# Kernel optimization log

Hardware: AMD Instinct MI355X
Metric: run time of the kernel (lower is better)

Reference implementation:

```python
import jax, jax.numpy as jnp
import numpy as np

N, E, H, C = 100000, 1600000, 4, 32  # nodes, edges, heads, per-head channels
F_IN, F_HID, F_OUT = 128, 32, 16
NEG_SLOPE = 0.2


def setup_inputs() -> dict:
    key = jax.random.key(0)
    ks = jax.random.split(key, 16)
    s = 0.05
    return {
        "x": jax.random.normal(ks[0], (N, F_IN), jnp.float32),
        "edge_index": jax.random.randint(ks[1], (2, E), 0, N, jnp.int32),
        "W0": jax.random.normal(ks[2], (F_IN, H * C), jnp.float32) * s,
        "att_src0": jax.random.normal(ks[3], (H, C), jnp.float32) * s,
        "att_dst0": jax.random.normal(ks[4], (H, C), jnp.float32) * s,
        "b0": jax.random.normal(ks[5], (H * C,), jnp.float32) * s,
        "W1": jax.random.normal(ks[6], (H * C, H * C), jnp.float32) * s,
        "att_src1": jax.random.normal(ks[7], (H, C), jnp.float32) * s,
        "att_dst1": jax.random.normal(ks[8], (H, C), jnp.float32) * s,
        "b1": jax.random.normal(ks[9], (H * C,), jnp.float32) * s,
        "Wm1": jax.random.normal(ks[10], (H * C, F_HID), jnp.float32) * s,
        "bm1": jax.random.normal(ks[11], (F_HID,), jnp.float32) * s,
        "Wm2": jax.random.normal(ks[12], (F_HID, F_OUT), jnp.float32) * s,
        "bm2": jax.random.normal(ks[13], (F_OUT,), jnp.float32) * s,
    }


def gat_layer(x, src, dst, W, att_src, att_dst, bias):
    n = x.shape[0]
    h = (x @ W).reshape(n, H, C)                       # [N,H,C]
    a_src = jnp.einsum("nhc,hc->nh", h, att_src)       # [N,H]
    a_dst = jnp.einsum("nhc,hc->nh", h, att_dst)       # [N,H]
    e = a_src[src] + a_dst[dst]                        # [E,H]
    e = jnp.where(e > 0, e, NEG_SLOPE * e)             # leaky_relu(0.2)
    m = jax.ops.segment_max(e, dst, num_segments=n)    # [N,H] segment softmax
    ee = jnp.exp(e - m[dst])
    z = jax.ops.segment_sum(ee, dst, num_segments=n)
    alpha = ee / z[dst]                                # [E,H]
    msg = alpha[:, :, None] * h[src]                   # [E,H,C]
    out = jax.ops.segment_sum(msg, dst, num_segments=n)  # [N,H,C]
    return out.reshape(n, H * C) + bias


def reference(x, edge_index, W0, att_src0, att_dst0, b0,
              W1, att_src1, att_dst1, b1, Wm1, bm1, Wm2, bm2):
    src, dst = edge_index[0], edge_index[1]
    x = jax.nn.relu(gat_layer(x, src, dst, W0, att_src0, att_dst0, b0))
    x = jax.nn.relu(gat_layer(x, src, dst, W1, att_src1, att_dst1, b1))
    x = jax.nn.relu(x @ Wm1 + bm1)
    return x @ Wm2 + bm2
```

## Files before the change

kernel.cpp:

```cpp
#include <hip/hip_runtime.h>
#include <hip/hip_bf16.h>

#define NEG 0.2f

typedef __attribute__((ext_vector_type(8))) short short8v;
typedef __attribute__((ext_vector_type(4))) float f32x4;

static __device__ __forceinline__ float bf2f(unsigned int u16){
  return __uint_as_float(u16 << 16);
}
static __device__ __forceinline__ unsigned short f2bf(float f){
  __hip_bfloat16 h = __float2bfloat16(f);
  return *reinterpret_cast<unsigned short*>(&h);
}

#define CHUNK 2048
#define PER_T 8


static __device__ __forceinline__ void bcount_body(
    const int* __restrict__ dst, int* __restrict__ bcnt, int E, int NB,
    int blk, int* lc)
{
  int t = threadIdx.x;
  int ebase = blk * CHUNK;
  for (int j=t; j<NB; j+=256) lc[j]=0;
  __syncthreads();
  #pragma unroll
  for (int k=0;k<PER_T;++k){
    int i = ebase + t + k*256;
    if (i < E) atomicAdd(&lc[dst[i] >> 8], 1);
  }
  __syncthreads();
  for (int j=t; j<NB; j+=256){
    int c = lc[j];
    if (c) atomicAdd(&bcnt[j], c);
  }
}

static __device__ __forceinline__ void binpass_body(
    const int* __restrict__ src, const int* __restrict__ dst,
    int* __restrict__ bfill, unsigned int* __restrict__ pairs, int E, int NB,
    int blk, int* lcnt, int* lbase)
{
  int t = threadIdx.x;
  int ebase = blk * CHUNK;
  for (int j=t; j<NB; j+=256) lcnt[j]=0;
  __syncthreads();
  unsigned int pv[PER_T]; int pb[PER_T];
  #pragma unroll
  for (int k=0;k<PER_T;++k){
    int i = ebase + t + k*256;
    pb[k] = -1;
    if (i < E){
      int d = dst[i];
      int s = src[i];
      pb[k] = d >> 8;
      pv[k] = ((unsigned int)s << 8) | (unsigned int)(d & 255);
      atomicAdd(&lcnt[pb[k]], 1);
    }
  }
  __syncthreads();
  for (int j=t; j<NB; j+=256){
    int c = lcnt[j];
    lbase[j] = c ? atomicAdd(&bfill[j], c) : 0;
    lcnt[j] = 0;
  }
  __syncthreads();
  #pragma unroll
  for (int k=0;k<PER_T;++k){
    if (pb[k] >= 0){
      int ofs = atomicAdd(&lcnt[pb[k]], 1);
      pairs[lbase[pb[k]] + ofs] = pv[k];
    }
  }
}

template<int IN_BF16>
static __device__ __forceinline__ void gemm_att_body(
    const void* __restrict__ xin_, const unsigned short* __restrict__ wt,
    const float* __restrict__ atts, const float* __restrict__ attd,
    unsigned short* __restrict__ hb, float* __restrict__ as_, float* __restrict__ ad_,
    int n, int blk, unsigned short* xls)
{
  int t = threadIdx.x;
  int base = blk*64;
  int nrem = n - base;
  if (IN_BF16){
    const uint4* Xb = reinterpret_cast<const uint4*>(xin_);
    #pragma unroll
    for (int j=0;j<4;++j){
      int i = t + j*256;
      int row = i >> 4, c16 = i & 15;
      uint4 v = (row < nrem) ? Xb[(size_t)(base+row)*16 + c16]
                             : make_uint4(0,0,0,0);
      int addr = row*256 + ((c16*16) ^ ((row&7)<<4));
      *reinterpret_cast<uint4*>(reinterpret_cast<char*>(xls) + addr) = v;
    }
  } else {
    const float4* X4 = reinterpret_cast<const float4*>(xin_);
    #pragma unroll
    for (int j=0;j<8;++j){
      int i = t + j*256;
      int row = i >> 5, cb = i & 31;
      float4 v = (row < nrem) ? X4[(size_t)(base+row)*32 + cb] : make_float4(0.f,0.f,0.f,0.f);
      unsigned int p0 = (unsigned int)f2bf(v.x) | ((unsigned int)f2bf(v.y)<<16);
      unsigned int p1 = (unsigned int)f2bf(v.z) | ((unsigned int)f2bf(v.w)<<16);
      int addr = row*256 + ((cb*8) ^ ((row&7)<<4));
      *reinterpret_cast<uint2*>(reinterpret_cast<char*>(xls) + addr) = make_uint2(p0,p1);
    }
  }
  __syncthreads();
  int w = t >> 6;
  int l = t & 63;
  int l15 = l & 15, l4 = l >> 4;
  int n0 = w*32;
  short8v bfr[2][4];
  #pragma unroll
  for (int nt=0;nt<2;++nt){
    const unsigned short* bp = wt + (size_t)(n0 + nt*16 + l15)*128 + l4*8;
    #pragma unroll
    for (int kk=0;kk<4;++kk)
      bfr[nt][kk] = *reinterpret_cast<const short8v*>(bp + kk*32);
  }
  f32x4 acc[4][2];
  #pragma unroll
  for (int mt=0;mt<4;++mt)
    #pragma unroll
    for (int nt=0;nt<2;++nt)
      acc[mt][nt] = (f32x4){0.f,0.f,0.f,0.f};
  #pragma unroll
  for (int kk=0;kk<4;++kk){
    short8v afr[4];
    #pragma unroll
    for (int mt=0;mt<4;++mt){
      int row = mt*16 + l15;
      int addr = row*256 + ((kk*64 + l4*16) ^ ((row&7)<<4));
      afr[mt] = *reinterpret_cast<const short8v*>(reinterpret_cast<char*>(xls) + addr);
    }
    #pragma unroll
    for (int mt=0;mt<4;++mt)
      #pragma unroll
      for (int nt=0;nt<2;++nt)
        acc[mt][nt] = __builtin_amdgcn_mfma_f32_16x16x32_bf16(afr[mt], bfr[nt][kk], acc[mt][nt], 0, 0, 0);
  }
  float av0 = atts[n0 + l15],    av1 = atts[n0 + 16 + l15];
  float dv0 = attd[n0 + l15],    dv1 = attd[n0 + 16 + l15];
  #pragma unroll
  for (int mt=0;mt<4;++mt){
    #pragma unroll
    for (int r=0;r<4;++r){
      float ps = acc[mt][0][r]*av0 + acc[mt][1][r]*av1;
      float pd = acc[mt][0][r]*dv0 + acc[mt][1][r]*dv1;
      ps += __shfl_xor(ps,1); ps += __shfl_xor(ps,2);
      ps += __shfl_xor(ps,4); ps += __shfl_xor(ps,8);
      pd += __shfl_xor(pd,1); pd += __shfl_xor(pd,2);
      pd += __shfl_xor(pd,4); pd += __shfl_xor(pd,8);
      int node = base + mt*16 + l4*4 + r;
      if (l15==0 && node < n){
        as_[node*4 + w] = ps;
        ad_[node*4 + w] = pd;
      }
    }
  }
  __syncthreads();
  #pragma unroll
  for (int mt=0;mt<4;++mt)
    #pragma unroll
    for (int nt=0;nt<2;++nt)
      #pragma unroll
      for (int r=0;r<4;++r){
        int row = mt*16 + l4*4 + r;
        int col = n0 + nt*16 + l15;
        xls[row*128 + col] = f2bf(acc[mt][nt][r]);
      }
  __syncthreads();
  const uint4* xsrc = reinterpret_cast<const uint4*>(xls);
  uint4* hdst = reinterpret_cast<uint4*>(hb + (size_t)base*128);
  #pragma unroll
  for (int j=0;j<4;++j){
    int i = t + j*256;
    int row = i >> 4;
    if (row < nrem) hdst[i] = xsrc[i];
  }
}


__global__ __launch_bounds__(256) void k_wconv_bcount(
    const float* __restrict__ W0, const float* __restrict__ W1,
    unsigned short* __restrict__ wt0, unsigned short* __restrict__ wt1,
    const int* __restrict__ dst, int* __restrict__ bcnt, int E, int NB)
{
  __shared__ int lc[512];
  int b = blockIdx.x;
  if (b < 128){
    const float* W = (b < 64) ? W0 : W1;
    unsigned short* wt = (b < 64) ? wt0 : wt1;
    int i = (b & 63)*256 + threadIdx.x;
    int k = i >> 7, nn = i & 127;
    wt[nn*128 + k] = f2bf(W[i]);
  } else {
    bcount_body(dst, bcnt, E, NB, b - 128, lc);
  }
}

__global__ __launch_bounds__(256) void k_bscan(
    const int* __restrict__ bcnt, int* __restrict__ bstart,
    int* __restrict__ bfill, int NB)
{
  __shared__ int sd[256];
  int t = threadIdx.x;
  int i0 = 2*t, i1 = 2*t+1;
  int v0 = (i0<NB) ? bcnt[i0] : 0;
  int v1 = (i1<NB) ? bcnt[i1] : 0;
  int s = v0+v1;
  sd[t]=s; __syncthreads();
  for (int off=1; off<256; off<<=1){
    int x = (t>=off) ? sd[t-off] : 0;
    __syncthreads();
    sd[t] += x;
    __syncthreads();
  }
  int ex = sd[t]-s;
  if (i0<=NB){ bstart[i0]=ex; if(i0<NB) bfill[i0]=ex; }
  ex += v0;
  if (i1<=NB){ bstart[i1]=ex; if(i1<NB) bfill[i1]=ex; }
}

__global__ __launch_bounds__(256) void k_gemm1_binpass(
    const float* __restrict__ xin, const unsigned short* __restrict__ wt,
    const float* __restrict__ atts, const float* __restrict__ attd,
    unsigned short* __restrict__ hb, float* __restrict__ as_, float* __restrict__ ad_,
    int n, int nG,
    const int* __restrict__ src, const int* __restrict__ dst,
    int* __restrict__ bfill, unsigned int* __restrict__ pairs, int E, int NB)
{
  __shared__ __align__(16) unsigned short xls[64*128];
  __shared__ int lcnt[512];
  __shared__ int lbase[512];
  int b = blockIdx.x;
  if (b < nG){
    gemm_att_body<0>(xin, wt, atts, attd, hb, as_, ad_, n, b, xls);
  } else {
    binpass_body(src, dst, bfill, pairs, E, NB, b - nG, lcnt, lbase);
  }
}

__global__ __launch_bounds__(256) void k_gemm2(
    const unsigned short* __restrict__ xin, const unsigned short* __restrict__ wt,
    const float* __restrict__ atts, const float* __restrict__ attd,
    unsigned short* __restrict__ hb, float* __restrict__ as_, float* __restrict__ ad_, int n)
{
  __shared__ __align__(16) unsigned short xls[64*128];
  gemm_att_body<1>(xin, wt, atts, attd, hb, as_, ad_, n, blockIdx.x, xls);
}

__global__ __launch_bounds__(256) void k_csr(
    const unsigned int* __restrict__ pairs, const int* __restrict__ bstart,
    int* __restrict__ rowptr, int* __restrict__ csr, int n)
{
  __shared__ int lc[256];
  __shared__ int sd[256];
  __shared__ int rp[257];
  int b = blockIdx.x;
  int base = b << 8;
  int t = threadIdx.x;
  int cnt = n - base; if (cnt > 256) cnt = 256;
  int beg = bstart[b], end = bstart[b+1];
  lc[t]=0; __syncthreads();
  for (int i = beg + t; i < end; i += 256)
    atomicAdd(&lc[pairs[i] & 255u], 1);
  __syncthreads();
  int v = lc[t];
  sd[t]=v; __syncthreads();
  for (int off=1; off<256; off<<=1){
    int x = (t>=off) ? sd[t-off] : 0;
    __syncthreads();
    sd[t] += x;
    __syncthreads();
  }
  rp[t+1] = beg + sd[t];
  if (t==0) rp[0] = beg;
  lc[t] = 0;
  __syncthreads();
  if (t < cnt) rowptr[base + t] = rp[t];
  if (t==0 && base + cnt == n) rowptr[n] = rp[cnt];
  for (int i = beg + t; i < end; i += 256){
    unsigned int p = pairs[i];
    int d = (int)(p & 255u);
    int ofs = atomicAdd(&lc[d], 1);
    csr[rp[d] + ofs] = (int)(p >> 8);
  }
}

__global__ __launch_bounds__(256) void k_aggr(
    const unsigned short* __restrict__ hb, const float* __restrict__ as_,
    const float* __restrict__ ad_, const int* __restrict__ rowptr,
    const int* __restrict__ csr, const float* __restrict__ bias,
    unsigned short* __restrict__ out, int n)
{
  int wid = (int)((blockIdx.x*(size_t)blockDim.x + threadIdx.x) >> 6);
  int lane = threadIdx.x & 63;
  if (wid >= n) return;
  int half = lane >> 5;
  int li   = lane & 31;
  int c0   = li*4;
  int head = li >> 3;
  float adn = ad_[wid*4 + head];
  int beg = rowptr[wid], end = rowptr[wid+1];
  int deg = end - beg;
  float4 acc = make_float4(0.f,0.f,0.f,0.f);
  float z = 0.f;
  int nfull = deg & ~7;
  int lim = beg + nfull;
  int i = beg + half*4;
  int s0=0,s1=0,s2=0,s3=0;
  if (i < lim){ s0=csr[i]; s1=csr[i+1]; s2=csr[i+2]; s3=csr[i+3]; }
  for (; i < lim; ){
    int ni = i + 8;
    int t0=0,t1=0,t2=0,t3=0;
    if (ni < lim){ t0=csr[ni]; t1=csr[ni+1]; t2=csr[ni+2]; t3=csr[ni+3]; }
    float e0 = as_[s0*4+head];
    float e1 = as_[s1*4+head];
    float e2 = as_[s2*4+head];
    float e3 = as_[s3*4+head];
    uint2 p0 = *reinterpret_cast<const uint2*>(hb + (size_t)s0*128 + c0);
    uint2 p1 = *reinterpret_cast<const uint2*>(hb + (size_t)s1*128 + c0);
    uint2 p2 = *reinterpret_cast<const uint2*>(hb + (size_t)s2*128 + c0);
    uint2 p3 = *reinterpret_cast<const uint2*>(hb + (size_t)s3*128 + c0);
    e0 += adn; e1 += adn; e2 += adn; e3 += adn;
    e0 = (e0>0.f)?e0:NEG*e0;
    e1 = (e1>0.f)?e1:NEG*e1;
    e2 = (e2>0.f)?e2:NEG*e2;
    e3 = (e3>0.f)?e3:NEG*e3;
    float x0 = __expf(e0);
    float x1 = __expf(e1);
    float x2 = __expf(e2);
    float x3 = __expf(e3);
    z += (x0+x1)+(x2+x3);
    acc.x = fmaf(x0, bf2f(p0.x & 0xffffu), acc.x);
    acc.y = fmaf(x0, bf2f(p0.x >> 16),     acc.y);
    acc.z = fmaf(x0, bf2f(p0.y & 0xffffu), acc.z);
    acc.w = fmaf(x0, bf2f(p0.y >> 16),     acc.w);
    acc.x = fmaf(x1, bf2f(p1.x & 0xffffu), acc.x);
    acc.y = fmaf(x1, bf2f(p1.x >> 16),     acc.y);
    acc.z = fmaf(x1, bf2f(p1.y & 0xffffu), acc.z);
    acc.w = fmaf(x1, bf2f(p1.y >> 16),     acc.w);
    acc.x = fmaf(x2, bf2f(p2.x & 0xffffu), acc.x);
    acc.y = fmaf(x2, bf2f(p2.x >> 16),     acc.y);
    acc.z = fmaf(x2, bf2f(p2.y & 0xffffu), acc.z);
    acc.w = fmaf(x2, bf2f(p2.y >> 16),     acc.w);
    acc.x = fmaf(x3, bf2f(p3.x & 0xffffu), acc.x);
    acc.y = fmaf(x3, bf2f(p3.x >> 16),     acc.y);
    acc.z = fmaf(x3, bf2f(p3.y & 0xffffu), acc.z);
    acc.w = fmaf(x3, bf2f(p3.y >> 16),     acc.w);
    i = ni; s0=t0; s1=t1; s2=t2; s3=t3;
  }
  for (int j = beg + nfull + half; j < end; j += 2){
    int s = csr[j];
    float e = as_[s*4+head] + adn;
    e = (e>0.f)?e:NEG*e;
    float ee = __expf(e);
    z += ee;
    uint2 pv = *reinterpret_cast<const uint2*>(hb + (size_t)s*128 + c0);
    acc.x = fmaf(ee, bf2f(pv.x & 0xffffu), acc.x);
    acc.y = fmaf(ee, bf2f(pv.x >> 16),     acc.y);
    acc.z = fmaf(ee, bf2f(pv.y & 0xffffu), acc.z);
    acc.w = fmaf(ee, bf2f(pv.y >> 16),     acc.w);
  }
  z     += __shfl_xor(z, 32);
  acc.x += __shfl_xor(acc.x, 32);
  acc.y += __shfl_xor(acc.y, 32);
  acc.z += __shfl_xor(acc.z, 32);
  acc.w += __shfl_xor(acc.w, 32);
  if (half == 0){
    float4 o;
    if (deg > 0){
      float rz = 1.f/z;
      o.x = fmaxf(fmaf(acc.x,rz,bias[c0  ]), 0.f);
      o.y = fmaxf(fmaf(acc.y,rz,bias[c0+1]), 0.f);
      o.z = fmaxf(fmaf(acc.z,rz,bias[c0+2]), 0.f);
      o.w = fmaxf(fmaf(acc.w,rz,bias[c0+3]), 0.f);
    } else {
      o.x = fmaxf(bias[c0  ], 0.f);
      o.y = fmaxf(bias[c0+1], 0.f);
      o.z = fmaxf(bias[c0+2], 0.f);
      o.w = fmaxf(bias[c0+3], 0.f);
    }
    unsigned int lo = (unsigned int)f2bf(o.x) | ((unsigned int)f2bf(o.y)<<16);
    unsigned int hi = (unsigned int)f2bf(o.z) | ((unsigned int)f2bf(o.w)<<16);
    *reinterpret_cast<uint2*>(out + (size_t)wid*128 + c0) = make_uint2(lo,hi);
  }
}

__global__ __launch_bounds__(256) void k_mlp(
    const unsigned short* __restrict__ xb, const float* __restrict__ Wm1, const float* __restrict__ bm1,
    const float* __restrict__ Wm2, const float* __restrict__ bm2,
    float* __restrict__ out, int n)
{
  __shared__ float xs[64*129];
  __shared__ float w1s[128*32];
  __shared__ float hs[64*33];
  __shared__ float w2s[32*16];
  __shared__ float b1s[32];
  __shared__ float b2s[16];
  int t = threadIdx.x;
  int base = blockIdx.x*64;
  const uint4* Xb = reinterpret_cast<const uint4*>(xb);
  #pragma unroll
  for (int j=0;j<4;++j){
    int i = t + j*256;
    int row = i >> 4, seg = i & 15;
    uint4 v = (base+row < n) ? Xb[(size_t)(base+row)*16 + seg] : make_uint4(0,0,0,0);
    float* xp = &xs[row*129 + seg*8];
    xp[0] = bf2f(v.x & 0xffffu); xp[1] = bf2f(v.x >> 16);
    xp[2] = bf2f(v.y & 0xffffu); xp[3] = bf2f(v.y >> 16);
    xp[4] = bf2f(v.z & 0xffffu); xp[5] = bf2f(v.z >> 16);
    xp[6] = bf2f(v.w & 0xffffu); xp[7] = bf2f(v.w >> 16);
  }
  for (int i=t; i<128*32; i+=256) w1s[i]=Wm1[i];
  for (int i=t; i<32*16;  i+=256) w2s[i]=Wm2[i];
  if (t<32) b1s[t]=bm1[t];
  if (t<16) b2s[t]=bm2[t];
  __syncthreads();
  int l = t&63, g = t>>6;
  float hid[8];
  #pragma unroll
  for (int j=0;j<8;++j) hid[j]=0.f;
  for (int k=0;k<128;++k){
    float xk = xs[l*129+k];
    #pragma unroll
    for (int j=0;j<8;++j) hid[j] = fmaf(xk, w1s[k*32 + g*8 + j], hid[j]);
  }
  #pragma unroll
  for (int j=0;j<8;++j) hs[l*33 + g*8 + j] = fmaxf(hid[j] + b1s[g*8+j], 0.f);
  __syncthreads();
  float o[4] = {0.f,0.f,0.f,0.f};
  for (int k=0;k<32;++k){
    float xv = hs[l*33+k];
    #pragma unroll
    for (int j=0;j<4;++j) o[j] = fmaf(xv, w2s[k*16 + g*4 + j], o[j]);
  }
  int node = base + l;
  if (node < n){
    #pragma unroll
    for (int j=0;j<4;++j) out[(size_t)node*16 + g*4 + j] = o[j] + b2s[g*4+j];
  }
}

extern "C" void kernel_launch(void* const* d_in, const int* in_sizes, int n_in,
                              void* d_out, int out_size, void* d_ws, size_t ws_size,
                              hipStream_t stream)
{
  const float* x   = (const float*)d_in[0];
  const int*   ei  = (const int*)  d_in[1];
  const float* W0  = (const float*)d_in[2];
  const float* as0 = (const float*)d_in[3];
  const float* ad0 = (const float*)d_in[4];
  const float* b0  = (const float*)d_in[5];
  const float* W1  = (const float*)d_in[6];
  const float* as1 = (const float*)d_in[7];
  const float* ad1 = (const float*)d_in[8];
  const float* b1  = (const float*)d_in[9];
  const float* Wm1 = (const float*)d_in[10];
  const float* bm1 = (const float*)d_in[11];
  const float* Wm2 = (const float*)d_in[12];
  const float* bm2 = (const float*)d_in[13];
  int N = in_sizes[0]/128;
  int E = in_sizes[1]/2;
  const int* srcI = ei;
  const int* dstI = ei + E;

  char* ws = (char*)d_ws;
  size_t off = 0;
  auto alloc = [&](size_t bytes)->void*{
    void* p = ws + off; off += (bytes + 255) & ~(size_t)255; return p;
  };
  unsigned short* hbuf = (unsigned short*)alloc((size_t)N*128*2);
  unsigned short* xbuf = (unsigned short*)alloc((size_t)N*128*2);
  float* asb   = (float*)alloc((size_t)N*4*4);
  float* adb   = (float*)alloc((size_t)N*4*4);
  int* rowptr  = (int*)alloc((size_t)(N+1)*4);
  int* bcnt    = (int*)alloc(2048);
  int* bstart  = (int*)alloc(2052);
  int* bfill   = (int*)alloc(2048);
  int* csr     = (int*)alloc((size_t)E*4);
  unsigned int* pairs = (unsigned int*)alloc((size_t)E*4);
  unsigned short* wt0 = (unsigned short*)alloc(128*128*2);
  unsigned short* wt1 = (unsigned short*)alloc(128*128*2);
  (void)ws_size; (void)n_in; (void)out_size;

  int NB = (N + 255) >> 8;
  int gC = (E + CHUNK - 1) / CHUNK;
  int gG = (N+63)/64;
  int gA = (int)(((size_t)N*64 + 255)/256);

  hipMemsetAsync(bcnt, 0, 2048, stream);
  k_wconv_bcount<<<128+gC,256,0,stream>>>(W0, W1, wt0, wt1, dstI, bcnt, E, NB);
  k_bscan       <<<1,256,0,stream>>>(bcnt, bstart, bfill, NB);
  k_gemm1_binpass<<<gG+gC,256,0,stream>>>(x, wt0, as0, ad0, hbuf, asb, adb, N, gG,
                                          srcI, dstI, bfill, pairs, E, NB);
  k_csr         <<<NB,256,0,stream>>>(pairs, bstart, rowptr, csr, N);
  k_aggr        <<<gA,256,0,stream>>>(hbuf, asb, adb, rowptr, csr, b0, xbuf, N);
  k_gemm2       <<<gG,256,0,stream>>>(xbuf, wt1, as1, ad1, hbuf, asb, adb, N);
  k_aggr        <<<gA,256,0,stream>>>(hbuf, asb, adb, rowptr, csr, b1, xbuf, N);
  k_mlp         <<<gG,256,0,stream>>>(xbuf, Wm1, bm1, Wm2, bm2, (float*)d_out, N);
}
```

Baseline: 286.9 us.

## Fuse GAT aggregation with following GEMM and with the MLP head

Layer-1 aggregation is fused with the layer-2 GEMM and attention projection, and layer-2 aggregation is fused with the two-layer MLP. Each block of 64 nodes aggregates into shared memory and then runs the next stage in place. This removes two launches and two round-trips of the intermediate N×128 bf16 buffer through global memory. The cost is fewer waves in flight for the latency-bound gather (64 nodes per 256-thread block done serially, 16 rows per wave) plus separate h/a buffers per layer. The MLP now reads its weights straight from global instead of staging them in LDS.

Result: slower. 362.8 us (+26.4%).

```diff
diff --git a/kernel.cpp b/kernel.cpp
--- a/kernel.cpp
+++ b/kernel.cpp
@@ -16,7 +16,6 @@
 
 #define CHUNK 2048
 #define PER_T 8
-
 
 static __device__ __forceinline__ void bcount_body(
     const int* __restrict__ dst, int* __restrict__ bcnt, int E, int NB,
@@ -76,241 +75,14 @@
   }
 }
 
-template<int IN_BF16>
-static __device__ __forceinline__ void gemm_att_body(
-    const void* __restrict__ xin_, const unsigned short* __restrict__ wt,
-    const float* __restrict__ atts, const float* __restrict__ attd,
-    unsigned short* __restrict__ hb, float* __restrict__ as_, float* __restrict__ ad_,
-    int n, int blk, unsigned short* xls)
-{
-  int t = threadIdx.x;
-  int base = blk*64;
-  int nrem = n - base;
-  if (IN_BF16){
-    const uint4* Xb = reinterpret_cast<const uint4*>(xin_);
-    #pragma unroll
-    for (int j=0;j<4;++j){
-      int i = t + j*256;
-      int row = i >> 4, c16 = i & 15;
-      uint4 v = (row < nrem) ? Xb[(size_t)(base+row)*16 + c16]
-                             : make_uint4(0,0,0,0);
-      int addr = row*256 + ((c16*16) ^ ((row&7)<<4));
-      *reinterpret_cast<uint4*>(reinterpret_cast<char*>(xls) + addr) = v;
-    }
-  } else {
-    const float4* X4 = reinterpret_cast<const float4*>(xin_);
-    #pragma unroll
-    for (int j=0;j<8;++j){
-      int i = t + j*256;
-      int row = i >> 5, cb = i & 31;
-      float4 v = (row < nrem) ? X4[(size_t)(base+row)*32 + cb] : make_float4(0.f,0.f,0.f,0.f);
-      unsigned int p0 = (unsigned int)f2bf(v.x) | ((unsigned int)f2bf(v.y)<<16);
-      unsigned int p1 = (unsigned int)f2bf(v.z) | ((unsigned int)f2bf(v.w)<<16);
-      int addr = row*256 + ((cb*8) ^ ((row&7)<<4));
-      *reinterpret_cast<uint2*>(reinterpret_cast<char*>(xls) + addr) = make_uint2(p0,p1);
-    }
-  }
-  __syncthreads();
-  int w = t >> 6;
-  int l = t & 63;
-  int l15 = l & 15, l4 = l >> 4;
-  int n0 = w*32;
-  short8v bfr[2][4];
-  #pragma unroll
-  for (int nt=0;nt<2;++nt){
-    const unsigned short* bp = wt + (size_t)(n0 + nt*16 + l15)*128 + l4*8;
-    #pragma unroll
-    for (int kk=0;kk<4;++kk)
-      bfr[nt][kk] = *reinterpret_cast<const short8v*>(bp + kk*32);
-  }
-  f32x4 acc[4][2];
-  #pragma unroll
-  for (int mt=0;mt<4;++mt)
-    #pragma unroll
-    for (int nt=0;nt<2;++nt)
-      acc[mt][nt] = (f32x4){0.f,0.f,0.f,0.f};
-  #pragma unroll
-  for (int kk=0;kk<4;++kk){
-    short8v afr[4];
-    #pragma unroll
-    for (int mt=0;mt<4;++mt){
-      int row = mt*16 + l15;
-      int addr = row*256 + ((kk*64 + l4*16) ^ ((row&7)<<4));
-      afr[mt] = *reinterpret_cast<const short8v*>(reinterpret_cast<char*>(xls) + addr);
-    }
-    #pragma unroll
-    for (int mt=0;mt<4;++mt)
-      #pragma unroll
-      for (int nt=0;nt<2;++nt)
-        acc[mt][nt] = __builtin_amdgcn_mfma_f32_16x16x32_bf16(afr[mt], bfr[nt][kk], acc[mt][nt], 0, 0, 0);
-  }
-  float av0 = atts[n0 + l15],    av1 = atts[n0 + 16 + l15];
-  float dv0 = attd[n0 + l15],    dv1 = attd[n0 + 16 + l15];
-  #pragma unroll
-  for (int mt=0;mt<4;++mt){
-    #pragma unroll
-    for (int r=0;r<4;++r){
-      float ps = acc[mt][0][r]*av0 + acc[mt][1][r]*av1;
-      float pd = acc[mt][0][r]*dv0 + acc[mt][1][r]*dv1;
-      ps += __shfl_xor(ps,1); ps += __shfl_xor(ps,2);
-      ps += __shfl_xor(ps,4); ps += __shfl_xor(ps,8);
-      pd += __shfl_xor(pd,1); pd += __shfl_xor(pd,2);
-      pd += __shfl_xor(pd,4); pd += __shfl_xor(pd,8);
-      int node = base + mt*16 + l4*4 + r;
-      if (l15==0 && node < n){
-        as_[node*4 + w] = ps;
-        ad_[node*4 + w] = pd;
-      }
-    }
-  }
-  __syncthreads();
-  #pragma unroll
-  for (int mt=0;mt<4;++mt)
-    #pragma unroll
-    for (int nt=0;nt<2;++nt)
-      #pragma unroll
-      for (int r=0;r<4;++r){
-        int row = mt*16 + l4*4 + r;
-        int col = n0 + nt*16 + l15;
-        xls[row*128 + col] = f2bf(acc[mt][nt][r]);
-      }
-  __syncthreads();
-  const uint4* xsrc = reinterpret_cast<const uint4*>(xls);
-  uint4* hdst = reinterpret_cast<uint4*>(hb + (size_t)base*128);
-  #pragma unroll
-  for (int j=0;j<4;++j){
-    int i = t + j*256;
-    int row = i >> 4;
-    if (row < nrem) hdst[i] = xsrc[i];
-  }
-}
-
-
-__global__ __launch_bounds__(256) void k_wconv_bcount(
-    const float* __restrict__ W0, const float* __restrict__ W1,
-    unsigned short* __restrict__ wt0, unsigned short* __restrict__ wt1,
-    const int* __restrict__ dst, int* __restrict__ bcnt, int E, int NB)
-{
-  __shared__ int lc[512];
-  int b = blockIdx.x;
-  if (b < 128){
-    const float* W = (b < 64) ? W0 : W1;
-    unsigned short* wt = (b < 64) ? wt0 : wt1;
-    int i = (b & 63)*256 + threadIdx.x;
-    int k = i >> 7, nn = i & 127;
-    wt[nn*128 + k] = f2bf(W[i]);
-  } else {
-    bcount_body(dst, bcnt, E, NB, b - 128, lc);
-  }
-}
-
-__global__ __launch_bounds__(256) void k_bscan(
-    const int* __restrict__ bcnt, int* __restrict__ bstart,
-    int* __restrict__ bfill, int NB)
-{
-  __shared__ int sd[256];
-  int t = threadIdx.x;
-  int i0 = 2*t, i1 = 2*t+1;
-  int v0 = (i0<NB) ? bcnt[i0] : 0;
-  int v1 = (i1<NB) ? bcnt[i1] : 0;
-  int s = v0+v1;
-  sd[t]=s; __syncthreads();
-  for (int off=1; off<256; off<<=1){
-    int x = (t>=off) ? sd[t-off] : 0;
-    __syncthreads();
-    sd[t] += x;
-    __syncthreads();
-  }
-  int ex = sd[t]-s;
-  if (i0<=NB){ bstart[i0]=ex; if(i0<NB) bfill[i0]=ex; }
-  ex += v0;
-  if (i1<=NB){ bstart[i1]=ex; if(i1<NB) bfill[i1]=ex; }
-}
-
-__global__ __launch_bounds__(256) void k_gemm1_binpass(
-    const float* __restrict__ xin, const unsigned short* __restrict__ wt,
-    const float* __restrict__ atts, const float* __restrict__ attd,
-    unsigned short* __restrict__ hb, float* __restrict__ as_, float* __restrict__ ad_,
-    int n, int nG,
-    const int* __restrict__ src, const int* __restrict__ dst,
-    int* __restrict__ bfill, unsigned int* __restrict__ pairs, int E, int NB)
-{
-  __shared__ __align__(16) unsigned short xls[64*128];
-  __shared__ int lcnt[512];
-  __shared__ int lbase[512];
-  int b = blockIdx.x;
-  if (b < nG){
-    gemm_att_body<0>(xin, wt, atts, attd, hb, as_, ad_, n, b, xls);
-  } else {
-    binpass_body(src, dst, bfill, pairs, E, NB, b - nG, lcnt, lbase);
-  }
-}
-
-__global__ __launch_bounds__(256) void k_gemm2(
-    const unsigned short* __restrict__ xin, const unsigned short* __restrict__ wt,
-    const float* __restrict__ atts, const float* __restrict__ attd,
-    unsigned short* __restrict__ hb, float* __restrict__ as_, float* __restrict__ ad_, int n)
-{
-  __shared__ __align__(16) unsigned short xls[64*128];
-  gemm_att_body<1>(xin, wt, atts, attd, hb, as_, ad_, n, blockIdx.x, xls);
-}
-
-__global__ __launch_bounds__(256) void k_csr(
-    const unsigned int* __restrict__ pairs, const int* __restrict__ bstart,
-    int* __restrict__ rowptr, int* __restrict__ csr, int n)
-{
-  __shared__ int lc[256];
-  __shared__ int sd[256];
-  __shared__ int rp[257];
-  int b = blockIdx.x;
-  int base = b << 8;
-  int t = threadIdx.x;
-  int cnt = n - base; if (cnt > 256) cnt = 256;
-  int beg = bstart[b], end = bstart[b+1];
-  lc[t]=0; __syncthreads();
-  for (int i = beg + t; i < end; i += 256)
-    atomicAdd(&lc[pairs[i] & 255u], 1);
-  __syncthreads();
-  int v = lc[t];
-  sd[t]=v; __syncthreads();
-  for (int off=1; off<256; off<<=1){
-    int x = (t>=off) ? sd[t-off] : 0;
-    __syncthreads();
-    sd[t] += x;
-    __syncthreads();
-  }
-  rp[t+1] = beg + sd[t];
-  if (t==0) rp[0] = beg;
-  lc[t] = 0;
-  __syncthreads();
-  if (t < cnt) rowptr[base + t] = rp[t];
-  if (t==0 && base + cnt == n) rowptr[n] = rp[cnt];
-  for (int i = beg + t; i < end; i += 256){
-    unsigned int p = pairs[i];
-    int d = (int)(p & 255u);
-    int ofs = atomicAdd(&lc[d], 1);
-    csr[rp[d] + ofs] = (int)(p >> 8);
-  }
-}
-
-__global__ __launch_bounds__(256) void k_aggr(
+static __device__ __forceinline__ float4 aggr_partial(
     const unsigned short* __restrict__ hb, const float* __restrict__ as_,
-    const float* __restrict__ ad_, const int* __restrict__ rowptr,
-    const int* __restrict__ csr, const float* __restrict__ bias,
-    unsigned short* __restrict__ out, int n)
-{
-  int wid = (int)((blockIdx.x*(size_t)blockDim.x + threadIdx.x) >> 6);
-  int lane = threadIdx.x & 63;
-  if (wid >= n) return;
-  int half = lane >> 5;
-  int li   = lane & 31;
-  int c0   = li*4;
-  int head = li >> 3;
-  float adn = ad_[wid*4 + head];
-  int beg = rowptr[wid], end = rowptr[wid+1];
-  int deg = end - beg;
+    float adn, const int* __restrict__ csr, int beg, int end,
+    int half, int head, int c0, float& zref)
+{
   float4 acc = make_float4(0.f,0.f,0.f,0.f);
   float z = 0.f;
+  int deg = end - beg;
   int nfull = deg & ~7;
   int lim = beg + nfull;
   int i = beg + half*4;
@@ -368,83 +140,447 @@
     acc.z = fmaf(ee, bf2f(pv.y & 0xffffu), acc.z);
     acc.w = fmaf(ee, bf2f(pv.y >> 16),     acc.w);
   }
-  z     += __shfl_xor(z, 32);
-  acc.x += __shfl_xor(acc.x, 32);
-  acc.y += __shfl_xor(acc.y, 32);
-  acc.z += __shfl_xor(acc.z, 32);
-  acc.w += __shfl_xor(acc.w, 32);
-  if (half == 0){
-    float4 o;
-    if (deg > 0){
-      float rz = 1.f/z;
-      o.x = fmaxf(fmaf(acc.x,rz,bias[c0  ]), 0.f);
-      o.y = fmaxf(fmaf(acc.y,rz,bias[c0+1]), 0.f);
-      o.z = fmaxf(fmaf(acc.z,rz,bias[c0+2]), 0.f);
-      o.w = fmaxf(fmaf(acc.w,rz,bias[c0+3]), 0.f);
-    } else {
-      o.x = fmaxf(bias[c0  ], 0.f);
-      o.y = fmaxf(bias[c0+1], 0.f);
-      o.z = fmaxf(bias[c0+2], 0.f);
-      o.w = fmaxf(bias[c0+3], 0.f);
-    }
-    unsigned int lo = (unsigned int)f2bf(o.x) | ((unsigned int)f2bf(o.y)<<16);
-    unsigned int hi = (unsigned int)f2bf(o.z) | ((unsigned int)f2bf(o.w)<<16);
-    *reinterpret_cast<uint2*>(out + (size_t)wid*128 + c0) = make_uint2(lo,hi);
-  }
-}
-
-__global__ __launch_bounds__(256) void k_mlp(
-    const unsigned short* __restrict__ xb, const float* __restrict__ Wm1, const float* __restrict__ bm1,
+  zref = z;
+  return acc;
+}
+
+template<int IN_BF16>
+static __device__ __forceinline__ void gemm_att_body(
+    const void* __restrict__ xin_, const unsigned short* __restrict__ wt,
+    const float* __restrict__ atts, const float* __restrict__ attd,
+    unsigned short* __restrict__ hb, float* __restrict__ as_, float* __restrict__ ad_,
+    int n, int blk, unsigned short* xls)
+{
+  int t = threadIdx.x;
+  int base = blk*64;
+  int nrem = n - base;
+  if (IN_BF16){
+    const uint4* Xb = reinterpret_cast<const uint4*>(xin_);
+    #pragma unroll
+    for (int j=0;j<4;++j){
+      int i = t + j*256;
+      int row = i >> 4, c16 = i & 15;
+      uint4 v = (row < nrem) ? Xb[(size_t)(base+row)*16 + c16]
+                             : make_uint4(0,0,0,0);
+      int addr = row*256 + ((c16*16) ^ ((row&7)<<4));
+      *reinterpret_cast<uint4*>(reinterpret_cast<char*>(xls) + addr) = v;
+    }
+  } else {
+    const float4* X4 = reinterpret_cast<const float4*>(xin_);
+    #pragma unroll
+    for (int j=0;j<8;++j){
+      int i = t + j*256;
+      int row = i >> 5, cb = i & 31;
+      float4 v = (row < nrem) ? X4[(size_t)(base+row)*32 + cb] : make_float4(0.f,0.f,0.f,0.f);
+      unsigned int p0 = (unsigned int)f2bf(v.x) | ((unsigned int)f2bf(v.y)<<16);
+      unsigned int p1 = (unsigned int)f2bf(v.z) | ((unsigned int)f2bf(v.w)<<16);
+      int addr = row*256 + ((cb*8) ^ ((row&7)<<4));
+      *reinterpret_cast<uint2*>(reinterpret_cast<char*>(xls) + addr) = make_uint2(p0,p1);
+    }
+  }
+  __syncthreads();
+  int w = t >> 6;
+  int l = t & 63;
+  int l15 = l & 15, l4 = l >> 4;
+  int n0 = w*32;
+  short8v bfr[2][4];
+  #pragma unroll
+  for (int nt=0;nt<2;++nt){
+    const unsigned short* bp = wt + (size_t)(n0 + nt*16 + l15)*128 + l4*8;
+    #pragma unroll
+    for (int kk=0;kk<4;++kk)
+      bfr[nt][kk] = *reinterpret_cast<const short8v*>(bp + kk*32);
+  }
+  f32x4 acc[4][2];
+  #pragma unroll
+  for (int mt=0;mt<4;++mt)
+    #pragma unroll
+    for (int nt=0;nt<2;++nt)
+      acc[mt][nt] = (f32x4){0.f,0.f,0.f,0.f};
+  #pragma unroll
+  for (int kk=0;kk<4;++kk){
+    short8v afr[4];
+    #pragma unroll
+    for (int mt=0;mt<4;++mt){
+      int row = mt*16 + l15;
+      int addr = row*256 + ((kk*64 + l4*16) ^ ((row&7)<<4));
+      afr[mt] = *reinterpret_cast<const short8v*>(reinterpret_cast<char*>(xls) + addr);
+    }
+    #pragma unroll
+    for (int mt=0;mt<4;++mt)
+      #pragma unroll
+      for (int nt=0;nt<2;++nt)
+        acc[mt][nt] = __builtin_amdgcn_mfma_f32_16x16x32_bf16(afr[mt], bfr[nt][kk], acc[mt][nt], 0, 0, 0);
+  }
+  float av0 = atts[n0 + l15],    av1 = atts[n0 + 16 + l15];
+  float dv0 = attd[n0 + l15],    dv1 = attd[n0 + 16 + l15];
+  #pragma unroll
+  for (int mt=0;mt<4;++mt){
+    #pragma unroll
+    for (int r=0;r<4;++r){
+      float ps = acc[mt][0][r]*av0 + acc[mt][1][r]*av1;
+      float pd = acc[mt][0][r]*dv0 + acc[mt][1][r]*dv1;
+      ps += __shfl_xor(ps,1); ps += __shfl_xor(ps,2);
+      ps += __shfl_xor(ps,4); ps += __shfl_xor(ps,8);
+      pd += __shfl_xor(pd,1); pd += __shfl_xor(pd,2);
+      pd += __shfl_xor(pd,4); pd += __shfl_xor(pd,8);
+      int node = base + mt*16 + l4*4 + r;
+      if (l15==0 && node < n){
+        as_[node*4 + w] = ps;
+        ad_[node*4 + w] = pd;
+      }
+    }
+  }
+  __syncthreads();
+  #pragma unroll
+  for (int mt=0;mt<4;++mt)
+    #pragma unroll
+    for (int nt=0;nt<2;++nt)
+      #pragma unroll
+      for (int r=0;r<4;++r){
+        int row = mt*16 + l4*4 + r;
+        int col = n0 + nt*16 + l15;
+        xls[row*128 + col] = f2bf(acc[mt][nt][r]);
+      }
+  __syncthreads();
+  const uint4* xsrc = reinterpret_cast<const uint4*>(xls);
+  uint4* hdst = reinterpret_cast<uint4*>(hb + (size_t)base*128);
+  #pragma unroll
+  for (int j=0;j<4;++j){
+    int i = t + j*256;
+    int row = i >> 4;
+    if (row < nrem) hdst[i] = xsrc[i];
+  }
+}
+
+
+__global__ __launch_bounds__(256) void k_wconv_bcount(
+    const float* __restrict__ W0, const float* __restrict__ W1,
+    unsigned short* __restrict__ wt0, unsigned short* __restrict__ wt1,
+    const int* __restrict__ dst, int* __restrict__ bcnt, int E, int NB)
+{
+  __shared__ int lc[512];
+  int b = blockIdx.x;
+  if (b < 128){
+    const float* W = (b < 64) ? W0 : W1;
+    unsigned short* wt = (b < 64) ? wt0 : wt1;
+    int i = (b & 63)*256 + threadIdx.x;
+    int k = i >> 7, nn = i & 127;
+    wt[nn*128 + k] = f2bf(W[i]);
+  } else {
+    bcount_body(dst, bcnt, E, NB, b - 128, lc);
+  }
+}
+
+__global__ __launch_bounds__(256) void k_bscan(
+    const int* __restrict__ bcnt, int* __restrict__ bstart,
+    int* __restrict__ bfill, int NB)
+{
+  __shared__ int sd[256];
+  int t = threadIdx.x;
+  int i0 = 2*t, i1 = 2*t+1;
+  int v0 = (i0<NB) ? bcnt[i0] : 0;
+  int v1 = (i1<NB) ? bcnt[i1] : 0;
+  int s = v0+v1;
+  sd[t]=s; __syncthreads();
+  for (int off=1; off<256; off<<=1){
+    int x = (t>=off) ? sd[t-off] : 0;
+    __syncthreads();
+    sd[t] += x;
+    __syncthreads();
+  }
+  int ex = sd[t]-s;
+  if (i0<=NB){ bstart[i0]=ex; if(i0<NB) bfill[i0]=ex; }
+  ex += v0;
+  if (i1<=NB){ bstart[i1]=ex; if(i1<NB) bfill[i1]=ex; }
+}
+
+__global__ __launch_bounds__(256) void k_gemm1_binpass(
+    const float* __restrict__ xin, const unsigned short* __restrict__ wt,
+    const float* __restrict__ atts, const float* __restrict__ attd,
+    unsigned short* __restrict__ hb, float* __restrict__ as_, float* __restrict__ ad_,
+    int n, int nG,
+    const int* __restrict__ src, const int* __restrict__ dst,
+    int* __restrict__ bfill, unsigned int* __restrict__ pairs, int E, int NB)
+{
+  __shared__ __align__(16) unsigned short xls[64*128];
+  __shared__ int lcnt[512];
+  __shared__ int lbase[512];
+  int b = blockIdx.x;
+  if (b < nG){
+    gemm_att_body<0>(xin, wt, atts, attd, hb, as_, ad_, n, b, xls);
+  } else {
+    binpass_body(src, dst, bfill, pairs, E, NB, b - nG, lcnt, lbase);
+  }
+}
+
+__global__ __launch_bounds__(256) void k_csr(
+    const unsigned int* __restrict__ pairs, const int* __restrict__ bstart,
+    int* __restrict__ rowptr, int* __restrict__ csr, int n)
+{
+  __shared__ int lc[256];
+  __shared__ int sd[256];
+  __shared__ int rp[257];
+  int b = blockIdx.x;
+  int base = b << 8;
+  int t = threadIdx.x;
+  int cnt = n - base; if (cnt > 256) cnt = 256;
+  int beg = bstart[b], end = bstart[b+1];
+  lc[t]=0; __syncthreads();
+  for (int i = beg + t; i < end; i += 256)
+    atomicAdd(&lc[pairs[i] & 255u], 1);
+  __syncthreads();
+  int v = lc[t];
+  sd[t]=v; __syncthreads();
+  for (int off=1; off<256; off<<=1){
+    int x = (t>=off) ? sd[t-off] : 0;
+    __syncthreads();
+    sd[t] += x;
+    __syncthreads();
+  }
+  rp[t+1] = beg + sd[t];
+  if (t==0) rp[0] = beg;
+  lc[t] = 0;
+  __syncthreads();
+  if (t < cnt) rowptr[base + t] = rp[t];
+  if (t==0 && base + cnt == n) rowptr[n] = rp[cnt];
+  for (int i = beg + t; i < end; i += 256){
+    unsigned int p = pairs[i];
+    int d = (int)(p & 255u);
+    int ofs = atomicAdd(&lc[d], 1);
+    csr[rp[d] + ofs] = (int)(p >> 8);
+  }
+}
+
+__global__ __launch_bounds__(256) void k_aggr_gemm(
+    const unsigned short* __restrict__ hb_in, const float* __restrict__ as_in,
+    const float* __restrict__ ad_in, const int* __restrict__ rowptr,
+    const int* __restrict__ csr, const float* __restrict__ bias,
+    const unsigned short* __restrict__ wt, const float* __restrict__ atts,
+    const float* __restrict__ attd, unsigned short* __restrict__ hb_out,
+    float* __restrict__ as_out, float* __restrict__ ad_out, int n)
+{
+  __shared__ __align__(16) unsigned short xls[64*128];
+  int t = threadIdx.x;
+  int w = t >> 6, lane = t & 63;
+  int base = blockIdx.x*64;
+  int nrem = n - base;
+  int half = lane >> 5, li = lane & 31;
+  int c0 = li*4, head = li >> 3;
+  float4 b4 = *reinterpret_cast<const float4*>(bias + c0);
+  for (int it=0; it<16; ++it){
+    int row = it*4 + w;
+    int node = base + row;
+    float4 acc = make_float4(0.f,0.f,0.f,0.f);
+    float z = 0.f;
+    int deg = 0;
+    if (node < n){
+      float adn = ad_in[node*4 + head];
+      int beg = rowptr[node], end = rowptr[node+1];
+      deg = end - beg;
+      acc = aggr_partial(hb_in, as_in, adn, csr, beg, end, half, head, c0, z);
+    }
+    z     += __shfl_xor(z, 32);
+    acc.x += __shfl_xor(acc.x, 32);
+    acc.y += __shfl_xor(acc.y, 32);
+    acc.z += __shfl_xor(acc.z, 32);
+    acc.w += __shfl_xor(acc.w, 32);
+    if (half == 0){
+      unsigned int lo = 0, hi = 0;
+      if (node < n){
+        float4 o;
+        if (deg > 0){
+          float rz = 1.f/z;
+          o.x = fmaxf(fmaf(acc.x,rz,b4.x), 0.f);
+          o.y = fmaxf(fmaf(acc.y,rz,b4.y), 0.f);
+          o.z = fmaxf(fmaf(acc.z,rz,b4.z), 0.f);
+          o.w = fmaxf(fmaf(acc.w,rz,b4.w), 0.f);
+        } else {
+          o.x = fmaxf(b4.x,0.f); o.y = fmaxf(b4.y,0.f);
+          o.z = fmaxf(b4.z,0.f); o.w = fmaxf(b4.w,0.f);
+        }
+        lo = (unsigned int)f2bf(o.x) | ((unsigned int)f2bf(o.y)<<16);
+        hi = (unsigned int)f2bf(o.z) | ((unsigned int)f2bf(o.w)<<16);
+      }
+      int addr = row*256 + ((li*8) ^ ((row&7)<<4));
+      *reinterpret_cast<uint2*>(reinterpret_cast<char*>(xls) + addr) = make_uint2(lo,hi);
+    }
+  }
+  __syncthreads();
+  int l15 = lane & 15, l4 = lane >> 4;
+  int n0 = w*32;
+  short8v bfr[2][4];
+  #pragma unroll
+  for (int nt=0;nt<2;++nt){
+    const unsigned short* bp = wt + (size_t)(n0 + nt*16 + l15)*128 + l4*8;
+    #pragma unroll
+    for (int kk=0;kk<4;++kk)
+      bfr[nt][kk] = *reinterpret_cast<const short8v*>(bp + kk*32);
+  }
+  f32x4 gacc[4][2];
+  #pragma unroll
+  for (int mt=0;mt<4;++mt)
+    #pragma unroll
+    for (int nt=0;nt<2;++nt)
+      gacc[mt][nt] = (f32x4){0.f,0.f,0.f,0.f};
+  #pragma unroll
+  for (int kk=0;kk<4;++kk){
+    short8v afr[4];
+    #pragma unroll
+    for (int mt=0;mt<4;++mt){
+      int row = mt*16 + l15;
+      int addr = row*256 + ((kk*64 + l4*16) ^ ((row&7)<<4));
+      afr[mt] = *reinterpret_cast<const short8v*>(reinterpret_cast<char*>(xls) + addr);
+    }
+    #pragma unroll
+    for (int mt=0;mt<4;++mt)
+      #pragma unroll
+      for (int nt=0;nt<2;++nt)
+        gacc[mt][nt] = __builtin_amdgcn_mfma_f32_16x16x32_bf16(afr[mt], bfr[nt][kk], gacc[mt][nt], 0, 0, 0);
+  }
+  float av0 = atts[n0 + l15],    av1 = atts[n0 + 16 + l15];
+  float dv0 = attd[n0 + l15],    dv1 = attd[n0 + 16 + l15];
+  #pragma unroll
+  for (int mt=0;mt<4;++mt){
+    #pragma unroll
+    for (int r=0;r<4;++r){
+      float ps = gacc[mt][0][r]*av0 + gacc[mt][1][r]*av1;
+      float pd = gacc[mt][0][r]*dv0 + gacc[mt][1][r]*dv1;
+      ps += __shfl_xor(ps,1); ps += __shfl_xor(ps,2);
+      ps += __shfl_xor(ps,4); ps += __shfl_xor(ps,8);
+      pd += __shfl_xor(pd,1); pd += __shfl_xor(pd,2);
+      pd += __shfl_xor(pd,4); pd += __shfl_xor(pd,8);
+      int node = base + mt*16 + l4*4 + r;
+      if (l15==0 && node < n){
+        as_out[node*4 + w] = ps;
+        ad_out[node*4 + w] = pd;
+      }
+    }
+  }
+  __syncthreads();
+  #pragma unroll
+  for (int mt=0;mt<4;++mt)
+    #pragma unroll
+    for (int nt=0;nt<2;++nt)
+      #pragma unroll
+      for (int r=0;r<4;++r){
+        int row = mt*16 + l4*4 + r;
+        int col = n0 + nt*16 + l15;
+        xls[row*128 + col] = f2bf(gacc[mt][nt][r]);
+      }
+  __syncthreads();
+  const uint4* xsrc = reinterpret_cast<const uint4*>(xls);
+  uint4* hdst = reinterpret_cast<uint4*>(hb_out + (size_t)base*128);
+  #pragma unroll
+  for (int j=0;j<4;++j){
+    int i = t + j*256;
+    int row = i >> 4;
+    if (row < nrem) hdst[i] = xsrc[i];
+  }
+}
+
+__global__ __launch_bounds__(256) void k_aggr_mlp(
+    const unsigned short* __restrict__ hb_in, const float* __restrict__ as_in,
+    const float* __restrict__ ad_in, const int* __restrict__ rowptr,
+    const int* __restrict__ csr, const float* __restrict__ bias,
+    const float* __restrict__ Wm1, const float* __restrict__ bm1,
     const float* __restrict__ Wm2, const float* __restrict__ bm2,
     float* __restrict__ out, int n)
 {
-  __shared__ float xs[64*129];
-  __shared__ float w1s[128*32];
+  __shared__ unsigned int xs[64*65];
   __shared__ float hs[64*33];
-  __shared__ float w2s[32*16];
-  __shared__ float b1s[32];
-  __shared__ float b2s[16];
   int t = threadIdx.x;
+  int w = t >> 6, lane = t & 63;
   int base = blockIdx.x*64;
-  const uint4* Xb = reinterpret_cast<const uint4*>(xb);
-  #pragma unroll
-  for (int j=0;j<4;++j){
-    int i = t + j*256;
-    int row = i >> 4, seg = i & 15;
-    uint4 v = (base+row < n) ? Xb[(size_t)(base+row)*16 + seg] : make_uint4(0,0,0,0);
-    float* xp = &xs[row*129 + seg*8];
-    xp[0] = bf2f(v.x & 0xffffu); xp[1] = bf2f(v.x >> 16);
-    xp[2] = bf2f(v.y & 0xffffu); xp[3] = bf2f(v.y >> 16);
-    xp[4] = bf2f(v.z & 0xffffu); xp[5] = bf2f(v.z >> 16);
-    xp[6] = bf2f(v.w & 0xffffu); xp[7] = bf2f(v.w >> 16);
-  }
-  for (int i=t; i<128*32; i+=256) w1s[i]=Wm1[i];
-  for (int i=t; i<32*16;  i+=256) w2s[i]=Wm2[i];
-  if (t<32) b1s[t]=bm1[t];
-  if (t<16) b2s[t]=bm2[t];
-  __syncthreads();
-  int l = t&63, g = t>>6;
+  int half = lane >> 5, li = lane & 31;
+  int c0 = li*4, head = li >> 3;
+  float4 b4 = *reinterpret_cast<const float4*>(bias + c0);
+  for (int it=0; it<16; ++it){
+    int row = it*4 + w;
+    int node = base + row;
+    float4 acc = make_float4(0.f,0.f,0.f,0.f);
+    float z = 0.f;
+    int deg = 0;
+    if (node < n){
+      float adn = ad_in[node*4 + head];
+      int beg = rowptr[node], end = rowptr[node+1];
+      deg = end - beg;
+      acc = aggr_partial(hb_in, as_in, adn, csr, beg, end, half, head, c0, z);
+    }
+    z     += __shfl_xor(z, 32);
+    acc.x += __shfl_xor(acc.x, 32);
+    acc.y += __shfl_xor(acc.y, 32);
+    acc.z += __shfl_xor(acc.z, 32);
+    acc.w += __shfl_xor(acc.w, 32);
+    if (half == 0){
+      unsigned int lo = 0, hi = 0;
+      if (node < n){
+        float4 o;
+        if (deg > 0){
+          float rz = 1.f/z;
+          o.x = fmaxf(fmaf(acc.x,rz,b4.x), 0.f);
+          o.y = fmaxf(fmaf(acc.y,rz,b4.y), 0.f);
+          o.z = fmaxf(fmaf(acc.z,rz,b4.z), 0.f);
+          o.w = fmaxf(fmaf(acc.w,rz,b4.w), 0.f);
+        } else {
+          o.x = fmaxf(b4.x,0.f); o.y = fmaxf(b4.y,0.f);
+          o.z = fmaxf(b4.z,0.f); o.w = fmaxf(b4.w,0.f);
+        }
+        lo = (unsigned int)f2bf(o.x) | ((unsigned int)f2bf(o.y)<<16);
+        hi = (unsigned int)f2bf(o.z) | ((unsigned int)f2bf(o.w)<<16);
+      }
+      xs[row*65 + li*2    ] = lo;
+      xs[row*65 + li*2 + 1] = hi;
+    }
+  }
+  __syncthreads();
+  int l = lane, g = w;
+  float4 bm1a = *reinterpret_cast<const float4*>(bm1 + g*8);
+  float4 bm1b = *reinterpret_cast<const float4*>(bm1 + g*8 + 4);
   float hid[8];
   #pragma unroll
   for (int j=0;j<8;++j) hid[j]=0.f;
-  for (int k=0;k<128;++k){
-    float xk = xs[l*129+k];
-    #pragma unroll
-    for (int j=0;j<8;++j) hid[j] = fmaf(xk, w1s[k*32 + g*8 + j], hid[j]);
-  }
-  #pragma unroll
-  for (int j=0;j<8;++j) hs[l*33 + g*8 + j] = fmaxf(hid[j] + b1s[g*8+j], 0.f);
-  __syncthreads();
-  float o[4] = {0.f,0.f,0.f,0.f};
+  for (int kk=0; kk<64; ++kk){
+    unsigned int pv = xs[l*65 + kk];
+    float x0 = bf2f(pv & 0xffffu);
+    float x1 = bf2f(pv >> 16);
+    const float* w1r = Wm1 + (kk*2)*32 + g*8;
+    float4 wa0 = *reinterpret_cast<const float4*>(w1r);
+    float4 wa1 = *reinterpret_cast<const float4*>(w1r + 4);
+    float4 wb0 = *reinterpret_cast<const float4*>(w1r + 32);
+    float4 wb1 = *reinterpret_cast<const float4*>(w1r + 36);
+    hid[0] = fmaf(x0, wa0.x, fmaf(x1, wb0.x, hid[0]));
+    hid[1] = fmaf(x0, wa0.y, fmaf(x1, wb0.y, hid[1]));
+    hid[2] = fmaf(x0, wa0.z, fmaf(x1, wb0.z, hid[2]));
+    hid[3] = fmaf(x0, wa0.w, fmaf(x1, wb0.w, hid[3]));
+    hid[4] = fmaf(x0, wa1.x, fmaf(x1, wb1.x, hid[4]));
+    hid[5] = fmaf(x0, wa1.y, fmaf(x1, wb1.y, hid[5]));
+    hid[6] = fmaf(x0, wa1.z, fmaf(x1, wb1.z, hid[6]));
+    hid[7] = fmaf(x0, wa1.w, fmaf(x1, wb1.w, hid[7]));
+  }
+  hs[l*33 + g*8 + 0] = fmaxf(hid[0] + bm1a.x, 0.f);
+  hs[l*33 + g*8 + 1] = fmaxf(hid[1] + bm1a.y, 0.f);
+  hs[l*33 + g*8 + 2] = fmaxf(hid[2] + bm1a.z, 0.f);
+  hs[l*33 + g*8 + 3] = fmaxf(hid[3] + bm1a.w, 0.f);
+  hs[l*33 + g*8 + 4] = fmaxf(hid[4] + bm1b.x, 0.f);
+  hs[l*33 + g*8 + 5] = fmaxf(hid[5] + bm1b.y, 0.f);
+  hs[l*33 + g*8 + 6] = fmaxf(hid[6] + bm1b.z, 0.f);
+  hs[l*33 + g*8 + 7] = fmaxf(hid[7] + bm1b.w, 0.f);
+  __syncthreads();
+  float o0=0.f,o1=0.f,o2=0.f,o3=0.f;
   for (int k=0;k<32;++k){
-    float xv = hs[l*33+k];
-    #pragma unroll
-    for (int j=0;j<4;++j) o[j] = fmaf(xv, w2s[k*16 + g*4 + j], o[j]);
+    float xv = hs[l*33 + k];
+    float4 w2 = *reinterpret_cast<const float4*>(Wm2 + k*16 + g*4);
+    o0 = fmaf(xv, w2.x, o0);
+    o1 = fmaf(xv, w2.y, o1);
+    o2 = fmaf(xv, w2.z, o2);
+    o3 = fmaf(xv, w2.w, o3);
   }
   int node = base + l;
   if (node < n){
-    #pragma unroll
-    for (int j=0;j<4;++j) out[(size_t)node*16 + g*4 + j] = o[j] + b2s[g*4+j];
+    float4 b2 = *reinterpret_cast<const float4*>(bm2 + g*4);
+    float4 ov = make_float4(o0+b2.x, o1+b2.y, o2+b2.z, o3+b2.w);
+    *reinterpret_cast<float4*>(out + (size_t)node*16 + g*4) = ov;
   }
 }
 
@@ -476,10 +612,12 @@
   auto alloc = [&](size_t bytes)->void*{
     void* p = ws + off; off += (bytes + 255) & ~(size_t)255; return p;
   };
-  unsigned short* hbuf = (unsigned short*)alloc((size_t)N*128*2);
-  unsigned short* xbuf = (unsigned short*)alloc((size_t)N*128*2);
-  float* asb   = (float*)alloc((size_t)N*4*4);
-  float* adb   = (float*)alloc((size_t)N*4*4);
+  unsigned short* h1buf = (unsigned short*)alloc((size_t)N*128*2);
+  unsigned short* h2buf = (unsigned short*)alloc((size_t)N*128*2);
+  float* as1b  = (float*)alloc((size_t)N*4*4);
+  float* ad1b  = (float*)alloc((size_t)N*4*4);
+  float* as2b  = (float*)alloc((size_t)N*4*4);
+  float* ad2b  = (float*)alloc((size_t)N*4*4);
   int* rowptr  = (int*)alloc((size_t)(N+1)*4);
   int* bcnt    = (int*)alloc(2048);
   int* bstart  = (int*)alloc(2052);
@@ -493,16 +631,15 @@
   int NB = (N + 255) >> 8;
   int gC = (E + CHUNK - 1) / CHUNK;
   int gG = (N+63)/64;
-  int gA = (int)(((size_t)N*64 + 255)/256);
 
   hipMemsetAsync(bcnt, 0, 2048, stream);
   k_wconv_bcount<<<128+gC,256,0,stream>>>(W0, W1, wt0, wt1, dstI, bcnt, E, NB);
   k_bscan       <<<1,256,0,stream>>>(bcnt, bstart, bfill, NB);
-  k_gemm1_binpass<<<gG+gC,256,0,stream>>>(x, wt0, as0, ad0, hbuf, asb, adb, N, gG,
+  k_gemm1_binpass<<<gG+gC,256,0,stream>>>(x, wt0, as0, ad0, h1buf, as1b, ad1b, N, gG,
                                           srcI, dstI, bfill, pairs, E, NB);
   k_csr         <<<NB,256,0,stream>>>(pairs, bstart, rowptr, csr, N);
-  k_aggr        <<<gA,256,0,stream>>>(hbuf, asb, adb, rowptr, csr, b0, xbuf, N);
-  k_gemm2       <<<gG,256,0,stream>>>(xbuf, wt1, as1, ad1, hbuf, asb, adb, N);
-  k_aggr        <<<gA,256,0,stream>>>(hbuf, asb, adb, rowptr, csr, b1, xbuf, N);
-  k_mlp         <<<gG,256,0,stream>>>(xbuf, Wm1, bm1, Wm2, bm2, (float*)d_out, N);
-}
+  k_aggr_gemm   <<<gG,256,0,stream>>>(h1buf, as1b, ad1b, rowptr, csr, b0,
+                                      wt1, as1, ad1, h2buf, as2b, ad2b, N);
+  k_aggr_mlp    <<<gG,256,0,stream>>>(h2buf, as2b, ad2b, rowptr, csr, b1,
+                                      Wm1, bm1, Wm2, bm2, (float*)d_out, N);
+}
```
